# Performance work log

Hardware: AMD Instinct MI355X
Metric: run time of the kernel (lower is better)

The kernel has to match this reference:

```python
import jax, jax.numpy as jnp
import numpy as np

N, E = 100000, 1600000
IN, HID, NCLS = 128, 128, 64


def setup_inputs() -> dict:
    key = jax.random.key(0)
    ks = jax.random.split(key, 8)
    x = jax.random.normal(ks[0], (N, IN), jnp.float32)
    edge_index = jax.random.randint(ks[1], (2, E), 0, N, dtype=jnp.int32)
    s1 = 1.0 / np.sqrt(IN)
    s2 = 1.0 / np.sqrt(HID)
    return {
        "x": x,
        "edge_index": edge_index,
        "Wl1": jax.random.uniform(ks[2], (IN, HID), jnp.float32, -s1, s1),
        "Wr1": jax.random.uniform(ks[3], (IN, HID), jnp.float32, -s1, s1),
        "b1": jnp.zeros((HID,), jnp.float32),
        "Wl2": jax.random.uniform(ks[4], (HID, NCLS), jnp.float32, -s2, s2),
        "Wr2": jax.random.uniform(ks[5], (HID, NCLS), jnp.float32, -s2, s2),
        "b2": jnp.zeros((NCLS,), jnp.float32),
    }


def _sage_conv(x, src, dst, inv_deg, Wl, Wr, b):
    # mean-aggregate neighbor features at each destination node (PyG SAGEConv)
    agg = jax.ops.segment_sum(x[src], dst, num_segments=N)  # [N, d]
    agg = agg * inv_deg[:, None]
    # out = lin_l(mean_j x_j) + lin_r(x_i); bias lives in lin_l
    return agg @ Wl + x @ Wr + b


def reference(x, edge_index, Wl1, Wr1, b1, Wl2, Wr2, b2):
    src, dst = edge_index[0], edge_index[1]
    deg = jax.ops.segment_sum(jnp.ones((E,), jnp.float32), dst, num_segments=N)
    inv_deg = 1.0 / jnp.maximum(deg, 1.0)
    h = _sage_conv(x, src, dst, inv_deg, Wl1, Wr1, b1)
    h = jax.nn.relu(h)
    # dropout is identity at inference (training=False)
    h = _sage_conv(h, src, dst, inv_deg, Wl2, Wr2, b2)
    return jax.nn.log_softmax(h, axis=1)
```

## Files before the change

kernel.cpp:

```cpp
#include <hip/hip_runtime.h>
#include <hip/hip_bf16.h>


typedef __attribute__((ext_vector_type(8))) short short8;
typedef __attribute__((ext_vector_type(4))) float f32x4;
typedef __attribute__((ext_vector_type(2))) float f32x2;

#define NPB 512
#define BCAP 16384
#define CHUNK 8192

__device__ __forceinline__ ushort f2bf(float f) {
    unsigned u = __float_as_uint(f);
    return (ushort)((u + 0x7fff + ((u >> 16) & 1)) >> 16);
}
__device__ __forceinline__ float bflo(unsigned v) { return __uint_as_float(v << 16); }
__device__ __forceinline__ float bfhi(unsigned v) { return __uint_as_float(v & 0xffff0000u); }
__device__ __forceinline__ unsigned pk4bf(float a, float b) {
    unsigned r;
    asm("v_cvt_pk_bf16_f32 %0, %1, %2" : "=v"(r) : "v"(a), "v"(b));
    return r;
}
__device__ __forceinline__ f32x2 shflx2(f32x2 v, int m) {
    f32x2 r; r[0] = __shfl_xor(v[0], m); r[1] = __shfl_xor(v[1], m); return r;
}

__device__ __forceinline__ void wfrag_one(const float* W, ushort* Wf, int i, int COLS) {
    int j = i & 7, m = (i >> 3) & 15, kc = (i >> 7) & 15, ct = i >> 11;
    Wf[i] = f2bf(W[(kc * 8 + j) * COLS + ct * 16 + m]);
}

__global__ void __launch_bounds__(256)
k1_scatter_cvtw(const int* __restrict__ src, const int* __restrict__ dst,
                int* __restrict__ bcount, unsigned* __restrict__ bbuf, int E, int NSC,
                const float* __restrict__ Wl1, const float* __restrict__ Wr1,
                const float* __restrict__ Wl2, const float* __restrict__ Wr2,
                ushort* __restrict__ Wf_l1, ushort* __restrict__ Wf_r1,
                ushort* __restrict__ Wf_l2, ushort* __restrict__ Wf_r2) {
    int tid = threadIdx.x;
    if ((int)blockIdx.x >= NSC) {
        int i = ((int)blockIdx.x - NSC) * 256 + tid;
        if (i < 16384)       wfrag_one(Wl1, Wf_l1, i, 128);
        else if (i < 32768)  wfrag_one(Wr1, Wf_r1, i - 16384, 128);
        else if (i < 40960)  wfrag_one(Wl2, Wf_l2, i - 32768, 64);
        else if (i < 49152)  wfrag_one(Wr2, Wf_r2, i - 40960, 64);
        return;
    }
    __shared__ unsigned entry[CHUNK];
    __shared__ unsigned char ebkt[CHUNK];
    __shared__ int lhist[256], lbase[256], lcur[256];
    lhist[tid] = 0;
    __syncthreads();
    int e0 = blockIdx.x * CHUNK;
    int cnt = min(CHUNK, E - e0);
    int nv = cnt >> 2;
    for (int t = tid; t < nv; t += 256) {
        int4 d4 = ((const int4*)(dst + e0))[t];
        int4 s4 = ((const int4*)(src + e0))[t];
        int i = t * 4;
        int b0 = d4.x >> 9, b1 = d4.y >> 9, b2 = d4.z >> 9, b3 = d4.w >> 9;
        entry[i + 0] = ((unsigned)s4.x << 9) | (unsigned)(d4.x & 511);
        entry[i + 1] = ((unsigned)s4.y << 9) | (unsigned)(d4.y & 511);
        entry[i + 2] = ((unsigned)s4.z << 9) | (unsigned)(d4.z & 511);
        entry[i + 3] = ((unsigned)s4.w << 9) | (unsigned)(d4.w & 511);
        ebkt[i + 0] = (unsigned char)b0; ebkt[i + 1] = (unsigned char)b1;
        ebkt[i + 2] = (unsigned char)b2; ebkt[i + 3] = (unsigned char)b3;
        atomicAdd(&lhist[b0], 1); atomicAdd(&lhist[b1], 1);
        atomicAdd(&lhist[b2], 1); atomicAdd(&lhist[b3], 1);
    }
    for (int i = (nv << 2) + tid; i < cnt; i += 256) {
        int d = dst[e0 + i], s = src[e0 + i];
        int b = d >> 9;
        entry[i] = ((unsigned)s << 9) | (unsigned)(d & 511);
        ebkt[i] = (unsigned char)b;
        atomicAdd(&lhist[b], 1);
    }
    __syncthreads();
    int h = lhist[tid];
    lbase[tid] = (h > 0) ? atomicAdd(&bcount[tid], h) : 0;
    lcur[tid] = 0;
    __syncthreads();
    for (int i = tid; i < cnt; i += 256) {
        int b = ebkt[i];
        int o = atomicAdd(&lcur[b], 1);
        bbuf[(long)b * BCAP + lbase[b] + o] = entry[i];
    }
}

template <int CTOT>
__device__ __forceinline__ void stage_weights(const ushort* __restrict__ Wfl,
                                              const ushort* __restrict__ Wfr,
                                              ushort* dst, int tid) {
    constexpr int HALF = CTOT / 2;
    constexpr int ITERS = (CTOT * 2) / 8192;
#pragma unroll
    for (int r = 0; r < ITERS; ++r) {
        int u = r * 4096 + tid * 8;
        const ushort* s = (u < HALF) ? (Wfl + u) : (Wfr + (u - HALF));
        *(short8*)(dst + u) = *(const short8*)s;
    }
}

template <int COLS, bool F32IN>
__device__ __forceinline__ void proj_body(int bid, int tid,
                            const void* __restrict__ xin,
                            const ushort* __restrict__ Wfl, const ushort* __restrict__ Wfr,
                            const float* __restrict__ bias,
                            unsigned char* __restrict__ p8, ushort* __restrict__ q, int N,
                            ushort* wsm) {
    constexpr int CT = COLS / 16;
    stage_weights<2 * COLS * 128>(Wfl, Wfr, wsm, tid);
    __syncthreads();
    const ushort* Wl = wsm;
    const ushort* Wr = wsm + COLS * 128;

    int wave = tid >> 6, lane = tid & 63;
    int quad = lane >> 4, m = lane & 15;
    long row0 = (long)bid * 128 + wave * 16;
    long node = row0 + m;
    long arow = (node < N) ? node : (N - 1);

    f32x4 accp[CT], accq[CT];
#pragma unroll
    for (int ct = 0; ct < CT; ++ct) { accp[ct] = (f32x4)0.0f; accq[ct] = (f32x4)0.0f; }

#pragma unroll
    for (int kk = 0; kk < 128; kk += 32) {
        short8 b;
        if (F32IN) {
            const float* xf = (const float*)xin + arow * 128 + kk + quad * 8;
            float4 f0 = *(const float4*)xf;
            float4 f1 = *(const float4*)(xf + 4);
            union { short8 s; unsigned u[4]; } bu;
            bu.u[0] = pk4bf(f0.x, f0.y);
            bu.u[1] = pk4bf(f0.z, f0.w);
            bu.u[2] = pk4bf(f1.x, f1.y);
            bu.u[3] = pk4bf(f1.z, f1.w);
            b = bu.s;
        } else {
            b = *(const short8*)((const ushort*)xin + arow * 128 + kk + quad * 8);
        }
        int kc = (kk >> 3) + quad;
#pragma unroll
        for (int ct = 0; ct < CT; ++ct) {
            int boff = ((ct * 16 + kc) * 16 + m) * 8;
            short8 al = *(const short8*)(Wl + boff);
            short8 ar = *(const short8*)(Wr + boff);
            accp[ct] = __builtin_amdgcn_mfma_f32_16x16x32_bf16(al, b, accp[ct], 0, 0, 0);
            accq[ct] = __builtin_amdgcn_mfma_f32_16x16x32_bf16(ar, b, accq[ct], 0, 0, 0);
        }
    }

    if (node < N) {
#pragma unroll
        for (int ct = 0; ct < CT; ++ct) {
            int c0 = ct * 16 + quad * 4;
            float4 bv = *(const float4*)(bias + c0);
            float q0 = accq[ct][0] + bv.x, q1 = accq[ct][1] + bv.y;
            float q2 = accq[ct][2] + bv.z, q3 = accq[ct][3] + bv.w;
            unsigned w = (unsigned)__builtin_amdgcn_cvt_pk_fp8_f32(accp[ct][0], accp[ct][1], 0, false);
            w = (unsigned)__builtin_amdgcn_cvt_pk_fp8_f32(accp[ct][2], accp[ct][3], (int)w, true);
            *(unsigned*)(p8 + node * COLS + c0) = w;
            uint2 qw; qw.x = pk4bf(q0, q1); qw.y = pk4bf(q2, q3);
            *(uint2*)(q + node * COLS + c0) = qw;
        }
    }
}

__global__ void __launch_bounds__(512, 4)
k2_csr_proj1(const unsigned* __restrict__ bbuf, const int* __restrict__ bcount,
             int* __restrict__ rsd,
             float* __restrict__ inv_deg, int* __restrict__ ssrc, int NBcsr, int N,
             const float* __restrict__ x,
             const ushort* __restrict__ Wfl, const ushort* __restrict__ Wfr,
             const float* __restrict__ bias,
             unsigned char* __restrict__ p8, ushort* __restrict__ q) {
    extern __shared__ char smem[];
    int tid = threadIdx.x;
    if ((int)blockIdx.x >= NBcsr) {
        proj_body<128, true>((int)blockIdx.x - NBcsr, tid, x, Wfl, Wfr, bias, p8, q, N,
                             (ushort*)smem);
        return;
    }
    int* sdeg = (int*)smem;
    int* lcur = sdeg + NPB;
    int* wsum = lcur + NPB;
    int b = blockIdx.x;
    int node0 = b * NPB;
    sdeg[tid] = 0;
    __syncthreads();
    int cnt = bcount[b];
    long base = (long)b * BCAP;
    const unsigned* bb = bbuf + base;
    int nv = cnt >> 2;
    for (int t = tid; t < nv; t += 512) {
        uint4 e = ((const uint4*)bb)[t];
        atomicAdd(&sdeg[e.x & 511], 1);
        atomicAdd(&sdeg[e.y & 511], 1);
        atomicAdd(&sdeg[e.z & 511], 1);
        atomicAdd(&sdeg[e.w & 511], 1);
    }
    for (int i = (nv << 2) + tid; i < cnt; i += 512)
        atomicAdd(&sdeg[bb[i] & 511], 1);
    __syncthreads();
    int lane = tid & 63, wv = tid >> 6;
    int c0 = sdeg[tid];
    int v = c0;
#pragma unroll
    for (int o = 1; o < 64; o <<= 1) {
        int t = __shfl_up(v, o);
        if (lane >= o) v += t;
    }
    if (lane == 63) wsum[wv] = v;
    __syncthreads();
    int add = 0;
    for (int w = 0; w < wv; ++w) add += wsum[w];
    int rs0 = v + add - c0;
    lcur[tid] = rs0;
    if (node0 + tid < N) {
        int2 rv; rv.x = (int)(base + rs0); rv.y = c0;
        *(int2*)(rsd + 2 * (node0 + tid)) = rv;
        inv_deg[node0 + tid] = 1.0f / (float)(c0 > 1 ? c0 : 1);
    }
    __syncthreads();
    for (int t = tid; t < nv; t += 512) {
        uint4 e = ((const uint4*)bb)[t];
        int p0 = atomicAdd(&lcur[e.x & 511], 1);
        int p1 = atomicAdd(&lcur[e.y & 511], 1);
        int p2 = atomicAdd(&lcur[e.z & 511], 1);
        int p3 = atomicAdd(&lcur[e.w & 511], 1);
        ssrc[base + p0] = (int)(e.x >> 9);
        ssrc[base + p1] = (int)(e.y >> 9);
        ssrc[base + p2] = (int)(e.z >> 9);
        ssrc[base + p3] = (int)(e.w >> 9);
    }
    for (int i = (nv << 2) + tid; i < cnt; i += 512) {
        unsigned w = bb[i];
        int pos = atomicAdd(&lcur[w & 511], 1);
        ssrc[base + pos] = (int)(w >> 9);
    }
}

__global__ void __launch_bounds__(256)
agg_relu_kernel(const unsigned char* __restrict__ p8,
                const ushort* __restrict__ q,
                const int* __restrict__ ssrc,
                const int* __restrict__ rsd,
                const float* __restrict__ inv_deg,
                ushort* __restrict__ hb, int N) {
    int wave = threadIdx.x >> 6, lane = threadIdx.x & 63;
    int n = blockIdx.x * 4 + wave;
    if (n >= N) return;
    int g = lane >> 5, lm = lane & 31;
    int2 rv = *(const int2*)(rsd + 2 * n);
    int start = rv.x, d = rv.y;
    float iv = inv_deg[n];
    uint2 qv = make_uint2(0u, 0u);
    if (g == 0) qv = *(const uint2*)(q + (long)n * 128 + lm * 4);
    const int* sp = ssrc + start;
    const unsigned char* pb = p8 + lm * 4;
    f32x2 a0 = (f32x2)0.f, a1 = (f32x2)0.f;
    int j = 0;
    for (; j + 16 <= d; j += 16) {
        int s0 = sp[j + g],      s1 = sp[j + 2 + g],  s2 = sp[j + 4 + g],  s3 = sp[j + 6 + g];
        int s4 = sp[j + 8 + g],  s5 = sp[j + 10 + g], s6 = sp[j + 12 + g], s7 = sp[j + 14 + g];
        unsigned v0 = *(const unsigned*)(pb + (long)s0 * 128);
        unsigned v1 = *(const unsigned*)(pb + (long)s1 * 128);
        unsigned v2 = *(const unsigned*)(pb + (long)s2 * 128);
        unsigned v3 = *(const unsigned*)(pb + (long)s3 * 128);
        unsigned v4 = *(const unsigned*)(pb + (long)s4 * 128);
        unsigned v5 = *(const unsigned*)(pb + (long)s5 * 128);
        unsigned v6 = *(const unsigned*)(pb + (long)s6 * 128);
        unsigned v7 = *(const unsigned*)(pb + (long)s7 * 128);
        a0 += __builtin_amdgcn_cvt_pk_f32_fp8((int)v0, false);
        a1 += __builtin_amdgcn_cvt_pk_f32_fp8((int)v0, true);
        a0 += __builtin_amdgcn_cvt_pk_f32_fp8((int)v1, false);
        a1 += __builtin_amdgcn_cvt_pk_f32_fp8((int)v1, true);
        a0 += __builtin_amdgcn_cvt_pk_f32_fp8((int)v2, false);
        a1 += __builtin_amdgcn_cvt_pk_f32_fp8((int)v2, true);
        a0 += __builtin_amdgcn_cvt_pk_f32_fp8((int)v3, false);
        a1 += __builtin_amdgcn_cvt_pk_f32_fp8((int)v3, true);
        a0 += __builtin_amdgcn_cvt_pk_f32_fp8((int)v4, false);
        a1 += __builtin_amdgcn_cvt_pk_f32_fp8((int)v4, true);
        a0 += __builtin_amdgcn_cvt_pk_f32_fp8((int)v5, false);
        a1 += __builtin_amdgcn_cvt_pk_f32_fp8((int)v5, true);
        a0 += __builtin_amdgcn_cvt_pk_f32_fp8((int)v6, false);
        a1 += __builtin_amdgcn_cvt_pk_f32_fp8((int)v6, true);
        a0 += __builtin_amdgcn_cvt_pk_f32_fp8((int)v7, false);
        a1 += __builtin_amdgcn_cvt_pk_f32_fp8((int)v7, true);
    }
    if (j + 8 <= d) {
        int s0 = sp[j + g], s1 = sp[j + 2 + g], s2 = sp[j + 4 + g], s3 = sp[j + 6 + g];
        unsigned v0 = *(const unsigned*)(pb + (long)s0 * 128);
        unsigned v1 = *(const unsigned*)(pb + (long)s1 * 128);
        unsigned v2 = *(const unsigned*)(pb + (long)s2 * 128);
        unsigned v3 = *(const unsigned*)(pb + (long)s3 * 128);
        a0 += __builtin_amdgcn_cvt_pk_f32_fp8((int)v0, false);
        a1 += __builtin_amdgcn_cvt_pk_f32_fp8((int)v0, true);
        a0 += __builtin_amdgcn_cvt_pk_f32_fp8((int)v1, false);
        a1 += __builtin_amdgcn_cvt_pk_f32_fp8((int)v1, true);
        a0 += __builtin_amdgcn_cvt_pk_f32_fp8((int)v2, false);
        a1 += __builtin_amdgcn_cvt_pk_f32_fp8((int)v2, true);
        a0 += __builtin_amdgcn_cvt_pk_f32_fp8((int)v3, false);
        a1 += __builtin_amdgcn_cvt_pk_f32_fp8((int)v3, true);
        j += 8;
    }
    if (j + 4 <= d) {
        int s0 = sp[j + g], s1 = sp[j + 2 + g];
        unsigned v0 = *(const unsigned*)(pb + (long)s0 * 128);
        unsigned v1 = *(const unsigned*)(pb + (long)s1 * 128);
        a0 += __builtin_amdgcn_cvt_pk_f32_fp8((int)v0, false);
        a1 += __builtin_amdgcn_cvt_pk_f32_fp8((int)v0, true);
        a0 += __builtin_amdgcn_cvt_pk_f32_fp8((int)v1, false);
        a1 += __builtin_amdgcn_cvt_pk_f32_fp8((int)v1, true);
        j += 4;
    }
    for (; j < d; j += 2) {
        int idx = j + g;
        int s = sp[idx < d ? idx : j];
        unsigned vv = *(const unsigned*)(pb + (long)s * 128);
        if (idx < d) {
            a0 += __builtin_amdgcn_cvt_pk_f32_fp8((int)vv, false);
            a1 += __builtin_amdgcn_cvt_pk_f32_fp8((int)vv, true);
        }
    }
    a0 += shflx2(a0, 32); a1 += shflx2(a1, 32);
    if (g == 0) {
        float h0 = fmaxf(a0[0] * iv + bflo(qv.x), 0.f);
        float h1 = fmaxf(a0[1] * iv + bfhi(qv.x), 0.f);
        float h2 = fmaxf(a1[0] * iv + bflo(qv.y), 0.f);
        float h3 = fmaxf(a1[1] * iv + bfhi(qv.y), 0.f);
        uint2 hw;
        hw.x = pk4bf(h0, h1); hw.y = pk4bf(h2, h3);
        *(uint2*)(hb + (long)n * 128 + lm * 4) = hw;
    }
}

__global__ void __launch_bounds__(512, 4)
proj2_kernel(const ushort* __restrict__ hb,
             const ushort* __restrict__ Wfl, const ushort* __restrict__ Wfr,
             const float* __restrict__ bias,
             unsigned char* __restrict__ u8, ushort* __restrict__ v, int N) {
    __shared__ ushort wsm[2 * 64 * 128];
    proj_body<64, false>((int)blockIdx.x, (int)threadIdx.x, hb, Wfl, Wfr, bias, u8, v, N,
                         wsm);
}

__global__ void __launch_bounds__(256)
agg_lsm_kernel(const unsigned char* __restrict__ u8,
               const ushort* __restrict__ v,
               const int* __restrict__ ssrc,
               const int* __restrict__ rsd,
               const float* __restrict__ inv_deg,
               float* __restrict__ out, int N) {
    int wave = threadIdx.x >> 6, lane = threadIdx.x & 63;
    int n = blockIdx.x * 4 + wave;
    if (n >= N) return;
    int g = lane >> 4, lm = lane & 15;
    int2 rv = *(const int2*)(rsd + 2 * n);
    int start = rv.x, d = rv.y;
    float iv = inv_deg[n];
    uint2 vv2 = *(const uint2*)(v + (long)n * 64 + lm * 4);
    const int* sp = ssrc + start;
    const unsigned char* ub = u8 + lm * 4;
    f32x2 a0 = (f32x2)0.f, a1 = (f32x2)0.f;
    int j = 0;
    for (; j + 16 <= d; j += 16) {
        int s0 = sp[j + g], s1 = sp[j + 4 + g], s2 = sp[j + 8 + g], s3 = sp[j + 12 + g];
        unsigned v0 = *(const unsigned*)(ub + (long)s0 * 64);
        unsigned v1 = *(const unsigned*)(ub + (long)s1 * 64);
        unsigned v2 = *(const unsigned*)(ub + (long)s2 * 64);
        unsigned v3 = *(const unsigned*)(ub + (long)s3 * 64);
        a0 += __builtin_amdgcn_cvt_pk_f32_fp8((int)v0, false);
        a1 += __builtin_amdgcn_cvt_pk_f32_fp8((int)v0, true);
        a0 += __builtin_amdgcn_cvt_pk_f32_fp8((int)v1, false);
        a1 += __builtin_amdgcn_cvt_pk_f32_fp8((int)v1, true);
        a0 += __builtin_amdgcn_cvt_pk_f32_fp8((int)v2, false);
        a1 += __builtin_amdgcn_cvt_pk_f32_fp8((int)v2, true);
        a0 += __builtin_amdgcn_cvt_pk_f32_fp8((int)v3, false);
        a1 += __builtin_amdgcn_cvt_pk_f32_fp8((int)v3, true);
    }
    if (j + 8 <= d) {
        int s0 = sp[j + g], s1 = sp[j + 4 + g];
        unsigned v0 = *(const unsigned*)(ub + (long)s0 * 64);
        unsigned v1 = *(const unsigned*)(ub + (long)s1 * 64);
        a0 += __builtin_amdgcn_cvt_pk_f32_fp8((int)v0, false);
        a1 += __builtin_amdgcn_cvt_pk_f32_fp8((int)v0, true);
        a0 += __builtin_amdgcn_cvt_pk_f32_fp8((int)v1, false);
        a1 += __builtin_amdgcn_cvt_pk_f32_fp8((int)v1, true);
        j += 8;
    }
    for (; j < d; j += 4) {
        int idx = j + g;
        int s = sp[idx < d ? idx : j];
        unsigned vv = *(const unsigned*)(ub + (long)s * 64);
        if (idx < d) {
            a0 += __builtin_amdgcn_cvt_pk_f32_fp8((int)vv, false);
            a1 += __builtin_amdgcn_cvt_pk_f32_fp8((int)vv, true);
        }
    }
    a0 += shflx2(a0, 16); a1 += shflx2(a1, 16);
    a0 += shflx2(a0, 32); a1 += shflx2(a1, 32);

    float z0 = a0[0] * iv + bflo(vv2.x), z1 = a0[1] * iv + bfhi(vv2.x);
    float z2 = a1[0] * iv + bflo(vv2.y), z3 = a1[1] * iv + bfhi(vv2.y);
    float mx = fmaxf(fmaxf(z0, z1), fmaxf(z2, z3));
#pragma unroll
    for (int o = 8; o > 0; o >>= 1) mx = fmaxf(mx, __shfl_xor(mx, o));
    float e = (__expf(z0 - mx) + __expf(z1 - mx)) + (__expf(z2 - mx) + __expf(z3 - mx));
#pragma unroll
    for (int o = 8; o > 0; o >>= 1) e += __shfl_xor(e, o);
    float ls = mx + __logf(e);
    if (g == 0) {
        float4 o0;
        o0.x = z0 - ls; o0.y = z1 - ls; o0.z = z2 - ls; o0.w = z3 - ls;
        *(float4*)(out + (long)n * 64 + lm * 4) = o0;
    }
}

extern "C" void kernel_launch(void* const* d_in, const int* in_sizes, int n_in,
                              void* d_out, int out_size, void* d_ws, size_t ws_size,
                              hipStream_t stream) {
    const float* x   = (const float*)d_in[0];
    const int*   ei  = (const int*)d_in[1];
    const float* Wl1 = (const float*)d_in[2];
    const float* Wr1 = (const float*)d_in[3];
    const float* b1  = (const float*)d_in[4];
    const float* Wl2 = (const float*)d_in[5];
    const float* Wr2 = (const float*)d_in[6];
    const float* b2  = (const float*)d_in[7];

    const int N = in_sizes[0] / 128;
    const int E = in_sizes[1] / 2;
    const int* src = ei;
    const int* dst = ei + E;
    const int NB = (N + NPB - 1) / NPB;
    const int NSC = (E + CHUNK - 1) / CHUNK;

    size_t off = 0;
    auto take = [&](size_t nbytes) -> void* {
        void* ptr = (void*)((char*)d_ws + off);
        off += (nbytes + 255) & ~(size_t)255;
        return ptr;
    };
    int*      bcount    = (int*)take((size_t)NB * 4);
    unsigned* bbuf      = (unsigned*)take((size_t)NB * BCAP * 4);
    int*      rsd       = (int*)take((size_t)N * 8);
    float*    inv_deg   = (float*)take((size_t)N * 4);
    int*      ssrc      = (int*)take((size_t)NB * BCAP * 4);
    unsigned char* p8   = (unsigned char*)take((size_t)N * 128);
    ushort*   q         = (ushort*)take((size_t)N * 128 * 2);
    ushort*   hb        = (ushort*)take((size_t)N * 128 * 2);
    ushort*   Wf_l1     = (ushort*)take(128 * 128 * 2);
    ushort*   Wf_r1     = (ushort*)take(128 * 128 * 2);
    ushort*   Wf_l2     = (ushort*)take(64 * 128 * 2);
    ushort*   Wf_r2     = (ushort*)take(64 * 128 * 2);
    unsigned char* u8 = p8;
    ushort*        v  = q;
    (void)ws_size; (void)n_in; (void)out_size;

    static bool attr_set = false;
    if (!attr_set) {
        hipFuncSetAttribute((const void*)k2_csr_proj1,
                            hipFuncAttributeMaxDynamicSharedMemorySize, 65536);
        attr_set = true;
    }

    hipMemsetAsync(bcount, 0, (size_t)NB * 4, stream);

    k1_scatter_cvtw<<<NSC + 192, 256, 0, stream>>>(src, dst, bcount, bbuf, E, NSC,
                                                   Wl1, Wr1, Wl2, Wr2,
                                                   Wf_l1, Wf_r1, Wf_l2, Wf_r2);

    int P1 = (N + 127) / 128;
    k2_csr_proj1<<<NB + P1, 512, 65536, stream>>>(bbuf, bcount, rsd, inv_deg,
                                                  ssrc, NB, N, x, Wf_l1, Wf_r1, b1, p8, q);

    agg_relu_kernel<<<(N + 3) / 4, 256, 0, stream>>>(p8, q, ssrc, rsd, inv_deg, hb, N);

    proj2_kernel<<<(N + 127) / 128, 512, 0, stream>>>(hb, Wf_l2, Wf_r2, b2, u8, v, N);
    agg_lsm_kernel<<<(N + 3) / 4, 256, 0, stream>>>(u8, v, ssrc, rsd, inv_deg,
                                                    (float*)d_out, N);
}
```

Baseline: 251.9 us.

## Widen gather loads and software-pipeline neighbor index prefetch in aggregation kernels

The layer-1 aggregation now has each lane read 8 fp8 features (uint2) instead of 4, so four 16-lane groups process four edges in parallel rather than two 32-lane groups. Both aggregation kernels replace the unrolled main loop and its ragged tails with one 16-edge loop. That loop prefetches the next iteration's source indices while the current feature gathers are in flight, and masks out-of-range edges to zero. The intent is to cut the dependent index-to-feature load latency and the tail-handling overhead. In exchange, low-degree nodes do wasted padded loads, and the accumulator registers and shuffle reductions grow.

```diff
diff --git a/kernel.cpp b/kernel.cpp
--- a/kernel.cpp
+++ b/kernel.cpp
@@ -251,88 +251,64 @@
     int wave = threadIdx.x >> 6, lane = threadIdx.x & 63;
     int n = blockIdx.x * 4 + wave;
     if (n >= N) return;
-    int g = lane >> 5, lm = lane & 31;
+    int g = lane >> 4, lm = lane & 15;
     int2 rv = *(const int2*)(rsd + 2 * n);
     int start = rv.x, d = rv.y;
     float iv = inv_deg[n];
-    uint2 qv = make_uint2(0u, 0u);
-    if (g == 0) qv = *(const uint2*)(q + (long)n * 128 + lm * 4);
+    uint4 qv = make_uint4(0u, 0u, 0u, 0u);
+    if (g == 0) qv = *(const uint4*)(q + (long)n * 128 + lm * 8);
     const int* sp = ssrc + start;
-    const unsigned char* pb = p8 + lm * 4;
-    f32x2 a0 = (f32x2)0.f, a1 = (f32x2)0.f;
-    int j = 0;
-    for (; j + 16 <= d; j += 16) {
-        int s0 = sp[j + g],      s1 = sp[j + 2 + g],  s2 = sp[j + 4 + g],  s3 = sp[j + 6 + g];
-        int s4 = sp[j + 8 + g],  s5 = sp[j + 10 + g], s6 = sp[j + 12 + g], s7 = sp[j + 14 + g];
-        unsigned v0 = *(const unsigned*)(pb + (long)s0 * 128);
-        unsigned v1 = *(const unsigned*)(pb + (long)s1 * 128);
-        unsigned v2 = *(const unsigned*)(pb + (long)s2 * 128);
-        unsigned v3 = *(const unsigned*)(pb + (long)s3 * 128);
-        unsigned v4 = *(const unsigned*)(pb + (long)s4 * 128);
-        unsigned v5 = *(const unsigned*)(pb + (long)s5 * 128);
-        unsigned v6 = *(const unsigned*)(pb + (long)s6 * 128);
-        unsigned v7 = *(const unsigned*)(pb + (long)s7 * 128);
-        a0 += __builtin_amdgcn_cvt_pk_f32_fp8((int)v0, false);
-        a1 += __builtin_amdgcn_cvt_pk_f32_fp8((int)v0, true);
-        a0 += __builtin_amdgcn_cvt_pk_f32_fp8((int)v1, false);
-        a1 += __builtin_amdgcn_cvt_pk_f32_fp8((int)v1, true);
-        a0 += __builtin_amdgcn_cvt_pk_f32_fp8((int)v2, false);
-        a1 += __builtin_amdgcn_cvt_pk_f32_fp8((int)v2, true);
-        a0 += __builtin_amdgcn_cvt_pk_f32_fp8((int)v3, false);
-        a1 += __builtin_amdgcn_cvt_pk_f32_fp8((int)v3, true);
-        a0 += __builtin_amdgcn_cvt_pk_f32_fp8((int)v4, false);
-        a1 += __builtin_amdgcn_cvt_pk_f32_fp8((int)v4, true);
-        a0 += __builtin_amdgcn_cvt_pk_f32_fp8((int)v5, false);
-        a1 += __builtin_amdgcn_cvt_pk_f32_fp8((int)v5, true);
-        a0 += __builtin_amdgcn_cvt_pk_f32_fp8((int)v6, false);
-        a1 += __builtin_amdgcn_cvt_pk_f32_fp8((int)v6, true);
-        a0 += __builtin_amdgcn_cvt_pk_f32_fp8((int)v7, false);
-        a1 += __builtin_amdgcn_cvt_pk_f32_fp8((int)v7, true);
-    }
-    if (j + 8 <= d) {
-        int s0 = sp[j + g], s1 = sp[j + 2 + g], s2 = sp[j + 4 + g], s3 = sp[j + 6 + g];
-        unsigned v0 = *(const unsigned*)(pb + (long)s0 * 128);
-        unsigned v1 = *(const unsigned*)(pb + (long)s1 * 128);
-        unsigned v2 = *(const unsigned*)(pb + (long)s2 * 128);
-        unsigned v3 = *(const unsigned*)(pb + (long)s3 * 128);
-        a0 += __builtin_amdgcn_cvt_pk_f32_fp8((int)v0, false);
-        a1 += __builtin_amdgcn_cvt_pk_f32_fp8((int)v0, true);
-        a0 += __builtin_amdgcn_cvt_pk_f32_fp8((int)v1, false);
-        a1 += __builtin_amdgcn_cvt_pk_f32_fp8((int)v1, true);
-        a0 += __builtin_amdgcn_cvt_pk_f32_fp8((int)v2, false);
-        a1 += __builtin_amdgcn_cvt_pk_f32_fp8((int)v2, true);
-        a0 += __builtin_amdgcn_cvt_pk_f32_fp8((int)v3, false);
-        a1 += __builtin_amdgcn_cvt_pk_f32_fp8((int)v3, true);
-        j += 8;
-    }
-    if (j + 4 <= d) {
-        int s0 = sp[j + g], s1 = sp[j + 2 + g];
-        unsigned v0 = *(const unsigned*)(pb + (long)s0 * 128);
-        unsigned v1 = *(const unsigned*)(pb + (long)s1 * 128);
-        a0 += __builtin_amdgcn_cvt_pk_f32_fp8((int)v0, false);
-        a1 += __builtin_amdgcn_cvt_pk_f32_fp8((int)v0, true);
-        a0 += __builtin_amdgcn_cvt_pk_f32_fp8((int)v1, false);
-        a1 += __builtin_amdgcn_cvt_pk_f32_fp8((int)v1, true);
-        j += 4;
-    }
-    for (; j < d; j += 2) {
-        int idx = j + g;
-        int s = sp[idx < d ? idx : j];
-        unsigned vv = *(const unsigned*)(pb + (long)s * 128);
-        if (idx < d) {
-            a0 += __builtin_amdgcn_cvt_pk_f32_fp8((int)vv, false);
-            a1 += __builtin_amdgcn_cvt_pk_f32_fp8((int)vv, true);
-        }
-    }
+    const unsigned char* pb = p8 + lm * 8;
+    int dm1 = (d > 0) ? d - 1 : 0;
+    f32x2 a0 = (f32x2)0.f, a1 = (f32x2)0.f, a2 = (f32x2)0.f, a3 = (f32x2)0.f;
+    int s0 = sp[min(g, dm1)],      s1 = sp[min(4 + g, dm1)];
+    int s2 = sp[min(8 + g, dm1)],  s3 = sp[min(12 + g, dm1)];
+    for (int j = 0; j < d; j += 16) {
+        uint2 v0 = *(const uint2*)(pb + (unsigned)s0 * 128u);
+        uint2 v1 = *(const uint2*)(pb + (unsigned)s1 * 128u);
+        uint2 v2 = *(const uint2*)(pb + (unsigned)s2 * 128u);
+        uint2 v3 = *(const uint2*)(pb + (unsigned)s3 * 128u);
+        int jn = j + 16;
+        s0 = sp[min(jn + g, dm1)];      s1 = sp[min(jn + 4 + g, dm1)];
+        s2 = sp[min(jn + 8 + g, dm1)];  s3 = sp[min(jn + 12 + g, dm1)];
+        if (j + g >= d)      { v0.x = 0u; v0.y = 0u; }
+        if (j + 4 + g >= d)  { v1.x = 0u; v1.y = 0u; }
+        if (j + 8 + g >= d)  { v2.x = 0u; v2.y = 0u; }
+        if (j + 12 + g >= d) { v3.x = 0u; v3.y = 0u; }
+        a0 += __builtin_amdgcn_cvt_pk_f32_fp8((int)v0.x, false);
+        a1 += __builtin_amdgcn_cvt_pk_f32_fp8((int)v0.x, true);
+        a2 += __builtin_amdgcn_cvt_pk_f32_fp8((int)v0.y, false);
+        a3 += __builtin_amdgcn_cvt_pk_f32_fp8((int)v0.y, true);
+        a0 += __builtin_amdgcn_cvt_pk_f32_fp8((int)v1.x, false);
+        a1 += __builtin_amdgcn_cvt_pk_f32_fp8((int)v1.x, true);
+        a2 += __builtin_amdgcn_cvt_pk_f32_fp8((int)v1.y, false);
+        a3 += __builtin_amdgcn_cvt_pk_f32_fp8((int)v1.y, true);
+        a0 += __builtin_amdgcn_cvt_pk_f32_fp8((int)v2.x, false);
+        a1 += __builtin_amdgcn_cvt_pk_f32_fp8((int)v2.x, true);
+        a2 += __builtin_amdgcn_cvt_pk_f32_fp8((int)v2.y, false);
+        a3 += __builtin_amdgcn_cvt_pk_f32_fp8((int)v2.y, true);
+        a0 += __builtin_amdgcn_cvt_pk_f32_fp8((int)v3.x, false);
+        a1 += __builtin_amdgcn_cvt_pk_f32_fp8((int)v3.x, true);
+        a2 += __builtin_amdgcn_cvt_pk_f32_fp8((int)v3.y, false);
+        a3 += __builtin_amdgcn_cvt_pk_f32_fp8((int)v3.y, true);
+    }
+    a0 += shflx2(a0, 16); a1 += shflx2(a1, 16);
+    a2 += shflx2(a2, 16); a3 += shflx2(a3, 16);
     a0 += shflx2(a0, 32); a1 += shflx2(a1, 32);
+    a2 += shflx2(a2, 32); a3 += shflx2(a3, 32);
     if (g == 0) {
         float h0 = fmaxf(a0[0] * iv + bflo(qv.x), 0.f);
         float h1 = fmaxf(a0[1] * iv + bfhi(qv.x), 0.f);
         float h2 = fmaxf(a1[0] * iv + bflo(qv.y), 0.f);
         float h3 = fmaxf(a1[1] * iv + bfhi(qv.y), 0.f);
-        uint2 hw;
+        float h4 = fmaxf(a2[0] * iv + bflo(qv.z), 0.f);
+        float h5 = fmaxf(a2[1] * iv + bfhi(qv.z), 0.f);
+        float h6 = fmaxf(a3[0] * iv + bflo(qv.w), 0.f);
+        float h7 = fmaxf(a3[1] * iv + bfhi(qv.w), 0.f);
+        uint4 hw;
         hw.x = pk4bf(h0, h1); hw.y = pk4bf(h2, h3);
-        *(uint2*)(hb + (long)n * 128 + lm * 4) = hw;
+        hw.z = pk4bf(h4, h5); hw.w = pk4bf(h6, h7);
+        *(uint4*)(hb + (long)n * 128 + lm * 8) = hw;
     }
 }
 
@@ -363,14 +339,22 @@
     uint2 vv2 = *(const uint2*)(v + (long)n * 64 + lm * 4);
     const int* sp = ssrc + start;
     const unsigned char* ub = u8 + lm * 4;
+    int dm1 = (d > 0) ? d - 1 : 0;
     f32x2 a0 = (f32x2)0.f, a1 = (f32x2)0.f;
-    int j = 0;
-    for (; j + 16 <= d; j += 16) {
-        int s0 = sp[j + g], s1 = sp[j + 4 + g], s2 = sp[j + 8 + g], s3 = sp[j + 12 + g];
-        unsigned v0 = *(const unsigned*)(ub + (long)s0 * 64);
-        unsigned v1 = *(const unsigned*)(ub + (long)s1 * 64);
-        unsigned v2 = *(const unsigned*)(ub + (long)s2 * 64);
-        unsigned v3 = *(const unsigned*)(ub + (long)s3 * 64);
+    int s0 = sp[min(g, dm1)],      s1 = sp[min(4 + g, dm1)];
+    int s2 = sp[min(8 + g, dm1)],  s3 = sp[min(12 + g, dm1)];
+    for (int j = 0; j < d; j += 16) {
+        unsigned v0 = *(const unsigned*)(ub + (unsigned)s0 * 64u);
+        unsigned v1 = *(const unsigned*)(ub + (unsigned)s1 * 64u);
+        unsigned v2 = *(const unsigned*)(ub + (unsigned)s2 * 64u);
+        unsigned v3 = *(const unsigned*)(ub + (unsigned)s3 * 64u);
+        int jn = j + 16;
+        s0 = sp[min(jn + g, dm1)];      s1 = sp[min(jn + 4 + g, dm1)];
+        s2 = sp[min(jn + 8 + g, dm1)];  s3 = sp[min(jn + 12 + g, dm1)];
+        if (j + g >= d)      v0 = 0u;
+        if (j + 4 + g >= d)  v1 = 0u;
+        if (j + 8 + g >= d)  v2 = 0u;
+        if (j + 12 + g >= d) v3 = 0u;
         a0 += __builtin_amdgcn_cvt_pk_f32_fp8((int)v0, false);
         a1 += __builtin_amdgcn_cvt_pk_f32_fp8((int)v0, true);
         a0 += __builtin_amdgcn_cvt_pk_f32_fp8((int)v1, false);
@@ -379,25 +363,6 @@
         a1 += __builtin_amdgcn_cvt_pk_f32_fp8((int)v2, true);
         a0 += __builtin_amdgcn_cvt_pk_f32_fp8((int)v3, false);
         a1 += __builtin_amdgcn_cvt_pk_f32_fp8((int)v3, true);
-    }
-    if (j + 8 <= d) {
-        int s0 = sp[j + g], s1 = sp[j + 4 + g];
-        unsigned v0 = *(const unsigned*)(ub + (long)s0 * 64);
-        unsigned v1 = *(const unsigned*)(ub + (long)s1 * 64);
-        a0 += __builtin_amdgcn_cvt_pk_f32_fp8((int)v0, false);
-        a1 += __builtin_amdgcn_cvt_pk_f32_fp8((int)v0, true);
-        a0 += __builtin_amdgcn_cvt_pk_f32_fp8((int)v1, false);
-        a1 += __builtin_amdgcn_cvt_pk_f32_fp8((int)v1, true);
-        j += 8;
-    }
-    for (; j < d; j += 4) {
-        int idx = j + g;
-        int s = sp[idx < d ? idx : j];
-        unsigned vv = *(const unsigned*)(ub + (long)s * 64);
-        if (idx < d) {
-            a0 += __builtin_amdgcn_cvt_pk_f32_fp8((int)vv, false);
-            a1 += __builtin_amdgcn_cvt_pk_f32_fp8((int)vv, true);
-        }
     }
     a0 += shflx2(a0, 16); a1 += shflx2(a1, 16);
     a0 += shflx2(a0, 32); a1 += shflx2(a1, 32);
```

Result: faster. 245.2 us (-2.7%).
